# Performance work log

Measured on AMD Instinct MI355X. Metric: run time of the kernel, lower is better.

The kernel has to match this reference:

```python
import jax, jax.numpy as jnp
import numpy as np

TAU_S = 5.0  # network_config['tau_s']; n_steps inferred from trailing dim


def psp(x, tau_s):
    """Leaky synaptic integrator along the last (time) axis.
    x: [B, C, H, W, T] -> syns: [B, C, H, W, T]
    syn_t = syn_{t-1} * (1 - 1/tau_s) + x_t ;  out_t = syn_t / tau_s
    """
    decay = 1.0 - 1.0 / tau_s
    xt = jnp.moveaxis(x, -1, 0)  # [T, B, C, H, W]

    def step(syn, inp):
        syn = syn * decay + inp
        return syn, syn / tau_s

    _, ys = jax.lax.scan(step, jnp.zeros_like(xt[0]), xt)
    return jnp.moveaxis(ys, 0, -1)  # [B, C, H, W, T]


def setup_inputs() -> dict:
    key = jax.random.key(0)
    k1, k2 = jax.random.split(key)
    B, C, H, W, T = 32, 256, 4, 4, 100
    outputs = jax.random.normal(k1, (B, C, H, W, T), dtype=jnp.float32)
    # target is a spike train in the original; uniform [0,1) floats keep the
    # same math and dtype (fill='rand' per input_specs)
    target = jax.random.uniform(k2, (B, C, H, W, T), dtype=jnp.float32)
    return {"outputs": outputs, "target": target}


def reference(outputs, target):
    # spike_kernel: delta = outputs - psp(target); loss = 0.5 * sum(delta^2)
    delta = outputs - psp(target, TAU_S)
    return 0.5 * jnp.sum(delta * delta)
```

## Files before the change

kernel.cpp:

```cpp
#include <hip/hip_runtime.h>


#define BLOCK 256
#define WPB   (BLOCK / 64)
#define G     8

constexpr double dpow(double b, int n) {
  double r = 1.0; for (int i = 0; i < n; ++i) r *= b; return r;
}
constexpr float K1  = (float)dpow(0.4096, 1);
constexpr float K2  = (float)dpow(0.4096, 2);
constexpr float K4  = (float)dpow(0.4096, 4);
constexpr float K8  = (float)dpow(0.4096, 8);
constexpr float K16 = (float)dpow(0.4096, 16);
constexpr float B0 = (float)(0.2 * dpow(0.8, 1));
constexpr float B1 = (float)(0.2 * dpow(0.8, 2));
constexpr float B2 = (float)(0.2 * dpow(0.8, 3));
constexpr float B3 = (float)(0.2 * dpow(0.8, 4));
constexpr float G4C = (float)(0.04 * (dpow(0.8, 2) + dpow(0.8, 4) +
                                      dpow(0.8, 6) + dpow(0.8, 8)));
constexpr float L2D4 = -1.2877123795494493f;

__global__ __launch_bounds__(BLOCK) void spike_loss_kernel(
    const float4* __restrict__ o4g, const float4* __restrict__ x4g,
    float* __restrict__ out) {
  const int t    = threadIdx.x;
  const int lane = t & 63;
  const int w    = t >> 6;
  const int W    = blockIdx.x * WPB + w;
  const size_t gs = (size_t)W * (G * 64);
  const int b    = (int)(gs % 25);

  const float Wl = exp2f((float)(lane + 1) * L2D4);
  int p = b + lane;
  p -= (p >= 75) ? 75 : (p >= 50) ? 50 : (p >= 25) ? 25 : 0;

  const float4* op = o4g + gs + lane;
  const float4* xp = x4g + gs + lane;

  float4 ov[G], xv[G];
#pragma unroll
  for (int g = 0; g < G; ++g) { ov[g] = op[g * 64]; xv[g] = xp[g * 64]; }

  float C = 0.f;
  if (b) {
    float pu = 0.f;
    if (lane < b) {
      float4 px = x4g[gs - b + lane];
      float u = px.x;
      u = fmaf(0.8f, u, px.y); u = fmaf(0.8f, u, px.z); u = fmaf(0.8f, u, px.w);
      pu = u * exp2f((float)(b - 1 - lane) * L2D4);
    }
#pragma unroll
    for (int off = 32; off; off >>= 1) pu += __shfl_xor(pu, off, 64);
    C = pu;
  }

  float loss = 0.f;
#pragma unroll
  for (int g = 0; g < G; ++g) {
    float u, a, abar, bbar;
    u = xv[g].x;                 a = fmaf(-0.2f, u, ov[g].x);
    abar = a * a;                bbar = a * B0;
    u = fmaf(0.8f, u, xv[g].y);  a = fmaf(-0.2f, u, ov[g].y);
    abar = fmaf(a, a, abar);     bbar = fmaf(a, B1, bbar);
    u = fmaf(0.8f, u, xv[g].z);  a = fmaf(-0.2f, u, ov[g].z);
    abar = fmaf(a, a, abar);     bbar = fmaf(a, B2, bbar);
    u = fmaf(0.8f, u, xv[g].w);  a = fmaf(-0.2f, u, ov[g].w);
    abar = fmaf(a, a, abar);     bbar = fmaf(a, B3, bbar);

    const int q = min(p, lane);
    float c = u, up;
    up = __shfl_up(c, 1, 64);  if (q >= 1)  c = fmaf(K1,  up, c);
    up = __shfl_up(c, 2, 64);  if (q >= 2)  c = fmaf(K2,  up, c);
    up = __shfl_up(c, 4, 64);  if (q >= 4)  c = fmaf(K4,  up, c);
    up = __shfl_up(c, 8, 64);  if (q >= 8)  c = fmaf(K8,  up, c);
    up = __shfl_up(c, 16, 64); if (q >= 16) c = fmaf(K16, up, c);
    if (p > lane) c = fmaf(Wl, C, c);
    float Cn = __shfl(c, 63, 64);
    up = __shfl_up(c, 1, 64);
    float sigma = (p > 0) ? (lane ? up : C) : 0.f;

    loss += fmaf(fmaf(G4C, sigma, -2.f * bbar), sigma, abar);

    C = Cn;
    p += 14; if (p >= 25) p -= 25;
  }

#pragma unroll
  for (int off = 32; off > 0; off >>= 1) loss += __shfl_down(loss, off, 64);

  __shared__ float wsum[WPB];
  if (lane == 0) wsum[w] = loss;
  __syncthreads();
  if (t == 0) {
    float v = (wsum[0] + wsum[1]) + (wsum[2] + wsum[3]);
    atomicAdd(out, 0.5f * v);
  }
}

extern "C" void kernel_launch(void* const* d_in, const int* in_sizes, int n_in,
                              void* d_out, int out_size, void* d_ws, size_t ws_size,
                              hipStream_t stream) {
  const float4* o4 = (const float4*)d_in[0];
  const float4* x4 = (const float4*)d_in[1];
  float* loss = (float*)d_out;

  const int grid = in_sizes[0] / (8 * 64 * 4 * WPB);

  hipLaunchKernelGGL(spike_loss_kernel, dim3(grid), dim3(BLOCK), 0, stream,
                     o4, x4, loss);
}
```

Measured before the change: 124.2 us.

## Give each wave 25 float4 groups with double-buffered chunked loads

Each wave now covers 25 groups of 64 float4s, a whole number of 100-step time series, so it always starts aligned. That removes the carry-in prefix computation that used to reread preceding data. Loads are split into chunks of 5 and double-buffered, so the next chunk's global reads overlap with the shuffle-based scan on the current chunk. The broadcast of lane 63 now uses readlane instead of a shuffle. The grid shrinks roughly threefold, which lowers parallelism and raises register use from the two chunk buffers.

```diff
diff --git a/kernel.cpp b/kernel.cpp
--- a/kernel.cpp
+++ b/kernel.cpp
@@ -3,7 +3,8 @@
 
 #define BLOCK 256
 #define WPB   (BLOCK / 64)
-#define G     8
+#define TPW   25
+#define CH    5
 
 constexpr double dpow(double b, int n) {
   double r = 1.0; for (int i = 0; i < n; ++i) r *= b; return r;
@@ -27,64 +28,66 @@
   const int t    = threadIdx.x;
   const int lane = t & 63;
   const int w    = t >> 6;
-  const int W    = blockIdx.x * WPB + w;
-  const size_t gs = (size_t)W * (G * 64);
-  const int b    = (int)(gs % 25);
+  const int Wv   = blockIdx.x * WPB + w;
+  const size_t gs = (size_t)Wv * (TPW * 64);
 
   const float Wl = exp2f((float)(lane + 1) * L2D4);
-  int p = b + lane;
-  p -= (p >= 75) ? 75 : (p >= 50) ? 50 : (p >= 25) ? 25 : 0;
+  int p = lane;
+  p -= (p >= 50) ? 50 : (p >= 25) ? 25 : 0;
 
   const float4* op = o4g + gs + lane;
   const float4* xp = x4g + gs + lane;
 
-  float4 ov[G], xv[G];
+  float4 xc[CH], oc[CH], xn[CH], on[CH];
 #pragma unroll
-  for (int g = 0; g < G; ++g) { ov[g] = op[g * 64]; xv[g] = xp[g * 64]; }
+  for (int j = 0; j < CH; ++j) { xc[j] = xp[j * 64]; oc[j] = op[j * 64]; }
 
   float C = 0.f;
-  if (b) {
-    float pu = 0.f;
-    if (lane < b) {
-      float4 px = x4g[gs - b + lane];
-      float u = px.x;
-      u = fmaf(0.8f, u, px.y); u = fmaf(0.8f, u, px.z); u = fmaf(0.8f, u, px.w);
-      pu = u * exp2f((float)(b - 1 - lane) * L2D4);
+  float loss = 0.f;
+#pragma unroll
+  for (int cb = 0; cb < TPW / CH; ++cb) {
+    if (cb < TPW / CH - 1) {
+#pragma unroll
+      for (int j = 0; j < CH; ++j) {
+        xn[j] = xp[((cb + 1) * CH + j) * 64];
+        on[j] = op[((cb + 1) * CH + j) * 64];
+      }
     }
 #pragma unroll
-    for (int off = 32; off; off >>= 1) pu += __shfl_xor(pu, off, 64);
-    C = pu;
-  }
+    for (int j = 0; j < CH; ++j) {
+      const float4 xv = xc[j], ov = oc[j];
+      float u, a, abar, bbar;
+      u = xv.x;                 a = fmaf(-0.2f, u, ov.x);
+      abar = a * a;             bbar = a * B0;
+      u = fmaf(0.8f, u, xv.y);  a = fmaf(-0.2f, u, ov.y);
+      abar = fmaf(a, a, abar);  bbar = fmaf(a, B1, bbar);
+      u = fmaf(0.8f, u, xv.z);  a = fmaf(-0.2f, u, ov.z);
+      abar = fmaf(a, a, abar);  bbar = fmaf(a, B2, bbar);
+      u = fmaf(0.8f, u, xv.w);  a = fmaf(-0.2f, u, ov.w);
+      abar = fmaf(a, a, abar);  bbar = fmaf(a, B3, bbar);
 
-  float loss = 0.f;
+      const int q = min(p, lane);
+      float c = u, up;
+      up = __shfl_up(c, 1, 64);  if (q >= 1)  c = fmaf(K1,  up, c);
+      up = __shfl_up(c, 2, 64);  if (q >= 2)  c = fmaf(K2,  up, c);
+      up = __shfl_up(c, 4, 64);  if (q >= 4)  c = fmaf(K4,  up, c);
+      up = __shfl_up(c, 8, 64);  if (q >= 8)  c = fmaf(K8,  up, c);
+      up = __shfl_up(c, 16, 64); if (q >= 16) c = fmaf(K16, up, c);
+      if (p > lane) c = fmaf(Wl, C, c);
+      const float Cn =
+          __int_as_float(__builtin_amdgcn_readlane(__float_as_int(c), 63));
+      up = __shfl_up(c, 1, 64);
+      const float sigma = (p > 0) ? (lane ? up : C) : 0.f;
+
+      loss += fmaf(fmaf(G4C, sigma, -2.f * bbar), sigma, abar);
+
+      C = Cn;
+      p += 14; if (p >= 25) p -= 25;
+    }
+    if (cb < TPW / CH - 1) {
 #pragma unroll
-  for (int g = 0; g < G; ++g) {
-    float u, a, abar, bbar;
-    u = xv[g].x;                 a = fmaf(-0.2f, u, ov[g].x);
-    abar = a * a;                bbar = a * B0;
-    u = fmaf(0.8f, u, xv[g].y);  a = fmaf(-0.2f, u, ov[g].y);
-    abar = fmaf(a, a, abar);     bbar = fmaf(a, B1, bbar);
-    u = fmaf(0.8f, u, xv[g].z);  a = fmaf(-0.2f, u, ov[g].z);
-    abar = fmaf(a, a, abar);     bbar = fmaf(a, B2, bbar);
-    u = fmaf(0.8f, u, xv[g].w);  a = fmaf(-0.2f, u, ov[g].w);
-    abar = fmaf(a, a, abar);     bbar = fmaf(a, B3, bbar);
-
-    const int q = min(p, lane);
-    float c = u, up;
-    up = __shfl_up(c, 1, 64);  if (q >= 1)  c = fmaf(K1,  up, c);
-    up = __shfl_up(c, 2, 64);  if (q >= 2)  c = fmaf(K2,  up, c);
-    up = __shfl_up(c, 4, 64);  if (q >= 4)  c = fmaf(K4,  up, c);
-    up = __shfl_up(c, 8, 64);  if (q >= 8)  c = fmaf(K8,  up, c);
-    up = __shfl_up(c, 16, 64); if (q >= 16) c = fmaf(K16, up, c);
-    if (p > lane) c = fmaf(Wl, C, c);
-    float Cn = __shfl(c, 63, 64);
-    up = __shfl_up(c, 1, 64);
-    float sigma = (p > 0) ? (lane ? up : C) : 0.f;
-
-    loss += fmaf(fmaf(G4C, sigma, -2.f * bbar), sigma, abar);
-
-    C = Cn;
-    p += 14; if (p >= 25) p -= 25;
+      for (int j = 0; j < CH; ++j) { xc[j] = xn[j]; oc[j] = on[j]; }
+    }
   }
 
 #pragma unroll
@@ -106,7 +109,7 @@
   const float4* x4 = (const float4*)d_in[1];
   float* loss = (float*)d_out;
 
-  const int grid = in_sizes[0] / (8 * 64 * 4 * WPB);
+  const int grid = in_sizes[0] / 25600;
 
   hipLaunchKernelGGL(spike_loss_kernel, dim3(grid), dim3(BLOCK), 0, stream,
                      o4, x4, loss);
```

Result: faster. 120.1 us (-3.3%).
